# Optimization experiments

Measured on AMD Instinct MI355X. Metric: run time of the kernel, lower is better.

## Reference

```python
import jax, jax.numpy as jnp
import numpy as np

B, L, E, H, HID, V, C = 256, 64, 300, 100, 200, 30000, 3


def setup_inputs() -> dict:
    key = jax.random.key(0)
    ks = jax.random.split(key, 20)
    rep1 = jax.random.randint(ks[0], (B, L), 0, V)
    rep2 = jax.random.randint(ks[1], (B, L), 0, V)
    len1 = jax.random.randint(ks[2], (B,), 1, L + 1)
    len2 = jax.random.randint(ks[3], (B,), 1, L + 1)
    ar = jnp.arange(L)
    mask1 = (ar[None, :] < len1[:, None]).astype(jnp.float32)
    mask2 = (ar[None, :] < len2[:, None]).astype(jnp.float32)
    emb = jax.random.normal(ks[4], (V, E), jnp.float32) * 0.1
    k = 1.0 / np.sqrt(H)
    u = lambda kk, s, a: jax.random.uniform(kk, s, jnp.float32, -a, a)
    W_ih1 = u(ks[5], (4 * H, E), k); W_hh1 = u(ks[6], (4 * H, H), k)
    b_ih1 = u(ks[7], (4 * H,), k);   b_hh1 = u(ks[8], (4 * H,), k)
    W_ih2 = u(ks[9], (4 * H, E), k); W_hh2 = u(ks[10], (4 * H, H), k)
    b_ih2 = u(ks[11], (4 * H,), k);  b_hh2 = u(ks[12], (4 * H,), k)
    # attention params: module inits uniform(-0.5, 0.5)
    Wy = u(ks[13], (H, H), 0.5); Wh = u(ks[14], (H, H), 0.5)
    Wr = u(ks[15], (H, H), 0.5); Wp = u(ks[16], (H, H), 0.5)
    aW = u(ks[17], (1, H), 0.5)
    k1 = 1.0 / np.sqrt(2 * H)
    W1 = u(ks[18], (HID, 2 * H), k1); b1 = u(ks[18], (HID,), k1)
    k2 = 1.0 / np.sqrt(HID)
    W2 = u(ks[19], (C, HID), k2); b2 = u(ks[19], (C,), k2)
    return {"rep1": rep1, "len1": len1, "mask1": mask1,
            "rep2": rep2, "len2": len2, "mask2": mask2,
            "emb": emb,
            "W_ih1": W_ih1, "W_hh1": W_hh1, "b_ih1": b_ih1, "b_hh1": b_hh1,
            "W_ih2": W_ih2, "W_hh2": W_hh2, "b_ih2": b_ih2, "b_hh2": b_hh2,
            "Wy": Wy, "Wh": Wh, "Wr": Wr, "Wp": Wp, "aW": aW,
            "W1": W1, "b1": b1, "W2": W2, "b2": b2}


def reference(rep1, len1, mask1, rep2, len2, mask2, emb,
              W_ih1, W_hh1, b_ih1, b_hh1, W_ih2, W_hh2, b_ih2, b_hh2,
              Wy, Wh, Wr, Wp, aW, W1, b1, W2, b2):
    Bb = rep1.shape[0]
    Hh = Wy.shape[0]
    bidx = jnp.arange(Bb)

    def run_lstm(sen, h0, c0, Wih, Whh, bih, bhh):
        # sen: [L, B, E]; PyTorch LSTM gate order i, f, g, o
        def step(carry, x):
            h, c = carry
            g = x @ Wih.T + bih + h @ Whh.T + bhh
            i, f, gg, o = jnp.split(g, 4, axis=-1)
            c = jax.nn.sigmoid(f) * c + jax.nn.sigmoid(i) * jnp.tanh(gg)
            h = jax.nn.sigmoid(o) * jnp.tanh(c)
            return (h, c), (h, c)
        _, (hs, cs) = jax.lax.scan(step, (h0, c0), sen)
        return hs, cs  # [L, B, H]

    def get_rep(sen1, sen2, l1, m1, l2):
        z = jnp.zeros((Bb, Hh), sen1.dtype)
        hs, cs = run_lstm(sen1, z, z, W_ih1, W_hh1, b_ih1, b_hh1)
        outp = hs.transpose(1, 0, 2)                      # [B, L, H]
        h0 = outp[bidx, l1 - 1]                           # last valid h
        c0 = cs.transpose(1, 0, 2)[bidx, l1 - 1]          # last valid c
        hs2, _ = run_lstm(sen2, h0, c0, W_ih2, W_hh2, b_ih2, b_hh2)
        lstm_outs = hs2.transpose(1, 0, 2)                # [B, L, H]
        WyY = outp @ Wy                                   # [B, L, H]
        a = aW[0]

        def ctx_step(cv, h_t):
            # h_t: [B, H]; recurrent Wr term on previous context vector
            WhH = (h_t @ Wh + cv @ Wr)[:, None, :] * m1[:, :, None]
            M = jnp.tanh(WyY + WhH)                       # [B, L, H]
            s = jnp.einsum('blh,h->bl', M, a)
            e = jnp.exp(s - s.max(1, keepdims=True)) * m1  # masked softmax numerator
            attn = e / e.sum(1, keepdims=True)
            cv_new = jnp.einsum('bl,blh->bh', attn, outp)
            return cv_new, cv_new

        _, cvs = jax.lax.scan(ctx_step, z, hs2)           # [L, B, H]
        cv = cvs.transpose(1, 0, 2)[bidx, l2 - 1]
        lo = lstm_outs[bidx, l2 - 1]
        return jnp.tanh(cv @ Wp + lo @ Wh)

    s1 = emb[rep1].transpose(1, 0, 2)   # [L, B, E]
    s2 = emb[rep2].transpose(1, 0, 2)
    f1 = get_rep(s1, s2, len1, mask1, len2)
    f2 = get_rep(s2, s1, len2, mask2, len1)
    final = jnp.concatenate([f1, f2], axis=1)             # [B, 2H]
    fc = jnp.tanh(final @ W1.T + b1)                      # dropout_rate = 0
    logits = fc @ W2.T + b2
    return jax.nn.log_softmax(logits, axis=1)
```

## Files before the change

### kernel.cpp

```cpp
#include <hip/hip_runtime.h>
#include <math.h>


__device__ __forceinline__ float sigf(float x) { return 1.f / (1.f + expf(-x)); }

__device__ __forceinline__ unsigned short f2b(float f) {
    unsigned int u = __float_as_uint(f);
    unsigned int r = (u + 0x7FFFu + ((u >> 16) & 1u)) >> 16;
    return (unsigned short)r;
}

typedef __attribute__((ext_vector_type(8))) short short8v;
typedef __attribute__((ext_vector_type(4))) float float4v;

__global__ void f32_to_bf16_kernel(const float* __restrict__ in,
                                   unsigned short* __restrict__ out, int n4)
{
    int i = blockIdx.x * blockDim.x + threadIdx.x;
    int stride = gridDim.x * blockDim.x;
    for (; i < n4; i += stride) {
        float4 v = ((const float4*)in)[i];
        ushort4 b;
        b.x = f2b(v.x); b.y = f2b(v.y); b.z = f2b(v.z); b.w = f2b(v.w);
        ((ushort4*)out)[i] = b;
    }
}

__global__ __launch_bounds__(256)
void gemm_xproj_mfma(const unsigned short* __restrict__ embb,
                     const int* __restrict__ repA, const int* __restrict__ repB,
                     const float* __restrict__ W,
                     const float* __restrict__ bias1, const float* __restrict__ bias2,
                     float* __restrict__ out)
{
    __shared__ __align__(16) unsigned short Afr[512 * 8];
    __shared__ __align__(16) unsigned short Bfr[320 * 8];
    int tid = threadIdx.x;
    int m0 = blockIdx.x * 128;
    int n0 = blockIdx.y * 80;
    int lane = tid & 63, wave = tid >> 6;

    int sA0 = tid * 2, sA1 = sA0 + 1;
    int lA0 = sA0 & 63, lA1 = sA1 & 63;
    int rA0 = m0 + (sA0 >> 6) * 16 + (lA0 & 15);
    int rA1 = m0 + (sA1 >> 6) * 16 + (lA1 & 15);
    int kgA0 = (lA0 >> 4) * 8, kgA1 = (lA1 >> 4) * 8;
    int tt0 = rA0 >> 9, bb0 = rA0 & 511;
    int tok0 = (bb0 < 256) ? repA[bb0 * 64 + tt0] : repB[(bb0 - 256) * 64 + tt0];
    int tt1 = rA1 >> 9, bb1 = rA1 & 511;
    int tok1 = (bb1 < 256) ? repA[bb1 * 64 + tt1] : repB[(bb1 - 256) * 64 + tt1];
    const unsigned short* pa0 = embb + (size_t)tok0 * 300 + kgA0;
    const unsigned short* pa1 = embb + (size_t)tok1 * 300 + kgA1;

    int sB0 = tid;
    int nB0 = n0 + (sB0 >> 6) * 16 + (sB0 & 15);
    int kgB0 = ((sB0 & 63) >> 4) * 8;
    const float* pb0 = W + (size_t)nB0 * 300 + kgB0;
    int nB1 = n0 + 64 + (tid & 15);
    int kgB1 = (tid >> 4) * 8;
    const float* pb1 = W + (size_t)nB1 * 300 + kgB1;

    float4v acc[2][5];
#pragma unroll
    for (int i = 0; i < 2; i++)
#pragma unroll
        for (int j = 0; j < 5; j++) acc[i][j] = (float4v){0.f, 0.f, 0.f, 0.f};

    for (int k0 = 0; k0 < 300; k0 += 32) {
        {
            unsigned short* d = &Afr[sA0 * 8];
            int kk = k0 + kgA0;
            if (kk + 8 <= 300) {
                *(ushort4*)d = *(const ushort4*)(pa0 + k0);
                *(ushort4*)(d + 4) = *(const ushort4*)(pa0 + k0 + 4);
            } else {
#pragma unroll
                for (int i = 0; i < 8; i++) d[i] = (kk + i < 300) ? pa0[k0 + i] : 0;
            }
        }
        {
            unsigned short* d = &Afr[sA1 * 8];
            int kk = k0 + kgA1;
            if (kk + 8 <= 300) {
                *(ushort4*)d = *(const ushort4*)(pa1 + k0);
                *(ushort4*)(d + 4) = *(const ushort4*)(pa1 + k0 + 4);
            } else {
#pragma unroll
                for (int i = 0; i < 8; i++) d[i] = (kk + i < 300) ? pa1[k0 + i] : 0;
            }
        }
        {
            unsigned short* d = &Bfr[sB0 * 8];
            int kk = k0 + kgB0;
            if (kk + 8 <= 300) {
                float4 lo = *(const float4*)(pb0 + k0);
                float4 hi = *(const float4*)(pb0 + k0 + 4);
                d[0] = f2b(lo.x); d[1] = f2b(lo.y); d[2] = f2b(lo.z); d[3] = f2b(lo.w);
                d[4] = f2b(hi.x); d[5] = f2b(hi.y); d[6] = f2b(hi.z); d[7] = f2b(hi.w);
            } else {
#pragma unroll
                for (int i = 0; i < 8; i++) d[i] = (kk + i < 300) ? f2b(pb0[k0 + i]) : 0;
            }
        }
        if (tid < 64) {
            unsigned short* d = &Bfr[(256 + tid) * 8];
            int kk = k0 + kgB1;
            if (kk + 8 <= 300) {
                float4 lo = *(const float4*)(pb1 + k0);
                float4 hi = *(const float4*)(pb1 + k0 + 4);
                d[0] = f2b(lo.x); d[1] = f2b(lo.y); d[2] = f2b(lo.z); d[3] = f2b(lo.w);
                d[4] = f2b(hi.x); d[5] = f2b(hi.y); d[6] = f2b(hi.z); d[7] = f2b(hi.w);
            } else {
#pragma unroll
                for (int i = 0; i < 8; i++) d[i] = (kk + i < 300) ? f2b(pb1[k0 + i]) : 0;
            }
        }
        __syncthreads();
        short8v a0 = ((const short8v*)Afr)[(wave * 2 + 0) * 64 + lane];
        short8v a1 = ((const short8v*)Afr)[(wave * 2 + 1) * 64 + lane];
#pragma unroll
        for (int nt = 0; nt < 5; nt++) {
            short8v b = ((const short8v*)Bfr)[nt * 64 + lane];
            acc[0][nt] = __builtin_amdgcn_mfma_f32_16x16x32_bf16(a0, b, acc[0][nt], 0, 0, 0);
            acc[1][nt] = __builtin_amdgcn_mfma_f32_16x16x32_bf16(a1, b, acc[1][nt], 0, 0, 0);
        }
        __syncthreads();
    }

    int rbase = (lane >> 4) * 4;
    int cbase = lane & 15;
#pragma unroll
    for (int mtl = 0; mtl < 2; mtl++) {
        int mt = wave * 2 + mtl;
#pragma unroll
        for (int nt = 0; nt < 5; nt++) {
            int col = n0 + nt * 16 + cbase;
            float bsum = bias1[col] + bias2[col];
#pragma unroll
            for (int r = 0; r < 4; r++) {
                int row = m0 + mt * 16 + rbase + r;
                out[(size_t)row * 400 + col] = acc[mtl][nt][r] + bsum;
            }
        }
    }
}

template<int TRANSB, int TRANSOUT>
__global__ void gemm_kernel(const float* __restrict__ A,
                            const float* __restrict__ Bm,
                            float* __restrict__ out, int M, int N, int K, int lda)
{
    __shared__ float As[8][132];
    __shared__ float Bs[8][132];
    int tid = threadIdx.x;
    int m0 = blockIdx.x * 128;
    int n0 = blockIdx.y * 128;
    int tx = tid & 15, ty = tid >> 4;
    float acc[8][8];
#pragma unroll
    for (int i = 0; i < 8; i++)
#pragma unroll
        for (int j = 0; j < 8; j++) acc[i][j] = 0.f;

    int mr = m0 + (tid >> 1);
    int p = tid & 1;
    const float* arow = A + (size_t)mr * lda;

    for (int k0 = 0; k0 < K; k0 += 8) {
        int kk = k0 + p * 4;
        float4 av = make_float4(0.f, 0.f, 0.f, 0.f);
        if (kk + 3 < K) {
            av = *(const float4*)(arow + kk);
        } else {
            float tmp[4] = {0.f, 0.f, 0.f, 0.f};
            for (int i = 0; i < 4; i++) if (kk + i < K) tmp[i] = arow[kk + i];
            av = make_float4(tmp[0], tmp[1], tmp[2], tmp[3]);
        }
        int ml = tid >> 1;
        As[p * 4 + 0][ml] = av.x; As[p * 4 + 1][ml] = av.y;
        As[p * 4 + 2][ml] = av.z; As[p * 4 + 3][ml] = av.w;

        {
            int kl = tid >> 5;
            int nc = (tid & 31) * 4;
            int krow = k0 + kl;
            float4 bv = make_float4(0.f, 0.f, 0.f, 0.f);
            if (krow < K) {
                if (n0 + nc + 3 < N) {
                    bv = *(const float4*)(Bm + (size_t)krow * N + n0 + nc);
                } else {
                    float tmp[4] = {0.f, 0.f, 0.f, 0.f};
                    for (int i = 0; i < 4; i++) if (n0 + nc + i < N) tmp[i] = Bm[(size_t)krow * N + n0 + nc + i];
                    bv = make_float4(tmp[0], tmp[1], tmp[2], tmp[3]);
                }
            }
            Bs[kl][nc + 0] = bv.x; Bs[kl][nc + 1] = bv.y;
            Bs[kl][nc + 2] = bv.z; Bs[kl][nc + 3] = bv.w;
        }
        __syncthreads();
#pragma unroll
        for (int k = 0; k < 8; k++) {
            float4 a0 = *(const float4*)&As[k][ty * 8];
            float4 a1 = *(const float4*)&As[k][ty * 8 + 4];
            float4 b0 = *(const float4*)&Bs[k][tx * 8];
            float4 b1 = *(const float4*)&Bs[k][tx * 8 + 4];
            float am[8] = {a0.x, a0.y, a0.z, a0.w, a1.x, a1.y, a1.z, a1.w};
            float bn[8] = {b0.x, b0.y, b0.z, b0.w, b1.x, b1.y, b1.z, b1.w};
#pragma unroll
            for (int i = 0; i < 8; i++)
#pragma unroll
                for (int j = 0; j < 8; j++) acc[i][j] += am[i] * bn[j];
        }
        __syncthreads();
    }

#pragma unroll
    for (int i = 0; i < 8; i++) {
        int m = m0 + ty * 8 + i;
#pragma unroll
        for (int j = 0; j < 8; j++) {
            int n = n0 + tx * 8 + j;
            if (n < N) {
                size_t oi;
                if (TRANSOUT) oi = ((size_t)(m >> 6) * N + n) * 64 + (m & 63);
                else oi = (size_t)m * N + n;
                out[oi] = acc[i][j];
            }
        }
    }
}

__global__ __launch_bounds__(512, 2)
void lstm_kernel(const float* __restrict__ X, const float* __restrict__ Whh,
                 const float* __restrict__ hs_prev, const float* __restrict__ cs_prev,
                 const int* __restrict__ len1, const int* __restrict__ len2,
                 float* __restrict__ hs_out, float* __restrict__ cs_out)
{
    int t = threadIdx.x;
    int b0 = blockIdx.x * 2, b1 = b0 + 1;
    __shared__ float4 h0s4[25], h1s4[25];
    __shared__ float g0s[400], g1s[400];
    float* h0s = (float*)h0s4;
    float* h1s = (float*)h1s4;

    float4 w[25];
    if (t < 400) {
        const float* wr = Whh + t * 100;
#pragma unroll
        for (int i = 0; i < 25; i++) w[i] = ((const float4*)wr)[i];
    }
    float c0r = 0.f, c1r = 0.f;
    if (hs_prev) {
        if (t < 100) {
            int la = (b0 < 256) ? len1[b0] : len2[b0 - 256];
            h0s[t] = hs_prev[(b0 * 64 + la - 1) * 100 + t];
            c0r = cs_prev[(b0 * 64 + la - 1) * 100 + t];
        } else if (t < 200) {
            int j = t - 100;
            int la = (b1 < 256) ? len1[b1] : len2[b1 - 256];
            h1s[j] = hs_prev[(b1 * 64 + la - 1) * 100 + j];
            c1r = cs_prev[(b1 * 64 + la - 1) * 100 + j];
        }
    } else {
        if (t < 100) h0s[t] = 0.f;
        else if (t < 200) h1s[t - 100] = 0.f;
    }
    __syncthreads();

    for (int ts = 0; ts < 64; ts++) {
        if (t < 400) {
            float x0 = X[(ts * 512 + b0) * 400 + t];
            float x1 = X[(ts * 512 + b1) * 400 + t];
            float acc0a = 0.f, acc1a = 0.f;
            float acc0b = 0.f, acc1b = 0.f;
#pragma unroll
            for (int i = 0; i < 25; i++) {
                float4 hv0 = h0s4[i], hv1 = h1s4[i];
                acc0a += w[i].x * hv0.x + w[i].y * hv0.y;
                acc0b += w[i].z * hv0.z + w[i].w * hv0.w;
                acc1a += w[i].x * hv1.x + w[i].y * hv1.y;
                acc1b += w[i].z * hv1.z + w[i].w * hv1.w;
            }
            g0s[t] = acc0a + acc0b + x0;
            g1s[t] = acc1a + acc1b + x1;
        }
        __syncthreads();
        if (t < 200) {
            int j = (t < 100) ? t : t - 100;
            const float* gs = (t < 100) ? g0s : g1s;
            float ig = sigf(gs[j]);
            float fg = sigf(gs[100 + j]);
            float gg = tanhf(gs[200 + j]);
            float og = sigf(gs[300 + j]);
            float c = (t < 100) ? c0r : c1r;
            c = fg * c + ig * gg;
            float h = og * tanhf(c);
            if (t < 100) {
                c0r = c; h0s[j] = h;
                hs_out[(b0 * 64 + ts) * 100 + j] = h;
                if (cs_out) cs_out[(b0 * 64 + ts) * 100 + j] = c;
            } else {
                c1r = c; h1s[j] = h;
                hs_out[(b1 * 64 + ts) * 100 + j] = h;
                if (cs_out) cs_out[(b1 * 64 + ts) * 100 + j] = c;
            }
        }
        __syncthreads();
    }
}

__global__ __launch_bounds__(256, 2)
void attn_fast(const float* __restrict__ WyYT, const float* __restrict__ outp,
               const float* __restrict__ WhH, const float* __restrict__ Wr,
               const float* __restrict__ Wp, const float* __restrict__ aW,
               const float* __restrict__ mask1, const float* __restrict__ mask2,
               const int* __restrict__ len1, const int* __restrict__ len2,
               float* __restrict__ rep)
{
    int t = threadIdx.x;
    int bg = blockIdx.x;
    __shared__ __align__(16) float wyy2[64][100];
    __shared__ float whq2[100];
    __shared__ float atl[64];
    __shared__ __align__(16) float ucv[104];
    __shared__ float den[2];
    __shared__ float csel[100];

    int j = t >> 1, half = t & 1;
    int l3 = t >> 2, q3 = t & 3;

    const float* wy = WyYT + (size_t)bg * 6400;
    for (int idx = t; idx < 6400; idx += 256)
        wyy2[idx & 63][idx >> 6] = 2.f * wy[idx];

    const float* ob = outp + (size_t)bg * 6400;
    float oreg[32];
    if (t < 200) {
#pragma unroll
        for (int i = 0; i < 32; i++)
            oreg[i] = ob[(half * 32 + i) * 100 + j];
    }
    float wrreg[50];
    if (t < 200) {
#pragma unroll
        for (int k = 0; k < 50; k++)
            wrreg[k] = Wr[(half * 50 + k) * 100 + j];
    }
    float a2r[25];
#pragma unroll
    for (int i = 0; i < 25; i++) a2r[i] = 2.f * aW[q3 * 25 + i];
    float sumA;
    {
        float p = 0.f;
#pragma unroll
        for (int i = 0; i < 25; i++) p += a2r[i];
        p += __shfl_xor(p, 1);
        p += __shfl_xor(p, 2);
        sumA = 0.5f * p;
    }
    float m3 = (bg < 256) ? mask1[bg * 64 + l3] : mask2[(bg - 256) * 64 + l3];
    int lenB = (bg < 256) ? len2[bg] : len1[bg - 256];

    if (t < 104) ucv[t] = 0.f;
    if (t < 2) den[t] = 0.5f;

    const float* whrow = WhH + (size_t)bg * 6400;
    float whc = (t < 200) ? whrow[j] : 0.f;
    float densel = 1.f, uselreg = 0.f;
    __syncthreads();

    for (int ts = 0; ts < 64; ts++) {
        if (t < 200) {
            float dsum = den[0] + den[1];
            if (ts == lenB) densel = dsum;
            float rd = __builtin_amdgcn_rcpf(dsum);
            float whn = (ts < 63) ? whrow[(ts + 1) * 100 + j] : 0.f;
            float p0 = 0.f, p1 = 0.f;
            const float2* uc2 = (const float2*)(ucv + half * 50);
#pragma unroll
            for (int i = 0; i < 25; i++) {
                float2 c = uc2[i];
                p0 += wrreg[2 * i] * c.x;
                p1 += wrreg[2 * i + 1] * c.y;
            }
            float comb = p0 + p1;
            comb += __shfl_xor(comb, 1);
            if (!half) whq2[j] = 2.f * (whc + comb * rd);
            whc = whn;
        }
        __syncthreads();
        {
            const float* wyr = &wyy2[l3][q3 * 25];
            const float* wqp = &whq2[q3 * 25];
            float neg = 0.f;
#pragma unroll
            for (int i = 0; i < 25; i++) {
                float arg = wyr[i] + m3 * wqp[i];
                neg += a2r[i] * __builtin_amdgcn_rcpf(__expf(arg) + 1.f);
            }
            neg += __shfl_xor(neg, 1);
            neg += __shfl_xor(neg, 2);
            float e = __expf(sumA - neg) * m3;
            if (q3 == 0) atl[l3] = e;
        }
        __syncthreads();
        if (t < 200) {
            const float* al = &atl[half * 32];
            float p0 = 0.f, p1 = 0.f;
#pragma unroll
            for (int i = 0; i < 16; i++) {
                p0 += al[2 * i] * oreg[2 * i];
                p1 += al[2 * i + 1] * oreg[2 * i + 1];
            }
            float comb = p0 + p1;
            comb += __shfl_xor(comb, 1);
            if (ts == lenB - 1) uselreg = comb;
            if (!half) ucv[j] = comb;
        } else if (t < 202) {
            int hh = t - 200;
            const float* al = &atl[hh * 32];
            float d = 0.f;
#pragma unroll
            for (int i = 0; i < 32; i++) d += al[i];
            den[hh] = d;
        }
        __syncthreads();
    }

    if (lenB == 64 && t < 200) densel = den[0] + den[1];
    if (t < 200 && !half) csel[j] = uselreg * __builtin_amdgcn_rcpf(densel);
    __syncthreads();
    if (t < 100) {
        float r = whrow[(lenB - 1) * 100 + t];
#pragma unroll
        for (int k = 0; k < 100; k++) r += csel[k] * Wp[k * 100 + t];
        rep[(size_t)bg * 100 + t] = tanhf(r);
    }
}

__global__ void final_kernel(const float* __restrict__ rep,
                             const float* __restrict__ W1, const float* __restrict__ b1,
                             const float* __restrict__ W2, const float* __restrict__ b2,
                             float* __restrict__ out)
{
    int b = blockIdx.x;
    int t = threadIdx.x;
    __shared__ float4 fin4[50];
    __shared__ float4 fc4[50];
    __shared__ float lg[3];
    float* fin = (float*)fin4;
    float* fc = (float*)fc4;
    if (t < 200) fin[t] = (t < 100) ? rep[b * 100 + t] : rep[(b + 256) * 100 + (t - 100)];
    __syncthreads();
    if (t < 200) {
        float acc = b1[t];
        const float4* w = (const float4*)(W1 + t * 200);
#pragma unroll
        for (int k = 0; k < 50; k++) {
            float4 wv = w[k];
            float4 fv = fin4[k];
            acc += wv.x * fv.x + wv.y * fv.y + wv.z * fv.z + wv.w * fv.w;
        }
        fc[t] = tanhf(acc);
    }
    __syncthreads();
    if (t < 3) {
        float acc = b2[t];
        const float4* w = (const float4*)(W2 + t * 200);
        for (int k = 0; k < 50; k++) {
            float4 wv = w[k];
            float4 fv = fc4[k];
            acc += wv.x * fv.x + wv.y * fv.y + wv.z * fv.z + wv.w * fv.w;
        }
        lg[t] = acc;
    }
    __syncthreads();
    if (t == 0) {
        float m = fmaxf(lg[0], fmaxf(lg[1], lg[2]));
        float s = expf(lg[0] - m) + expf(lg[1] - m) + expf(lg[2] - m);
        float lse = m + logf(s);
        out[b * 3 + 0] = lg[0] - lse;
        out[b * 3 + 1] = lg[1] - lse;
        out[b * 3 + 2] = lg[2] - lse;
    }
}

extern "C" void kernel_launch(void* const* d_in, const int* in_sizes, int n_in,
                              void* d_out, int out_size, void* d_ws, size_t ws_size,
                              hipStream_t stream)
{
    const int*   rep1  = (const int*)d_in[0];
    const int*   len1  = (const int*)d_in[1];
    const float* mask1 = (const float*)d_in[2];
    const int*   rep2  = (const int*)d_in[3];
    const int*   len2  = (const int*)d_in[4];
    const float* mask2 = (const float*)d_in[5];
    const float* emb   = (const float*)d_in[6];
    const float* W_ih1 = (const float*)d_in[7];
    const float* W_hh1 = (const float*)d_in[8];
    const float* b_ih1 = (const float*)d_in[9];
    const float* b_hh1 = (const float*)d_in[10];
    const float* W_ih2 = (const float*)d_in[11];
    const float* W_hh2 = (const float*)d_in[12];
    const float* b_ih2 = (const float*)d_in[13];
    const float* b_hh2 = (const float*)d_in[14];
    const float* Wy    = (const float*)d_in[15];
    const float* Wh    = (const float*)d_in[16];
    const float* Wr    = (const float*)d_in[17];
    const float* Wp    = (const float*)d_in[18];
    const float* aW    = (const float*)d_in[19];
    const float* W1    = (const float*)d_in[20];
    const float* b1    = (const float*)d_in[21];
    const float* W2    = (const float*)d_in[22];
    const float* b2    = (const float*)d_in[23];

    float* ws = (float*)d_ws;
    float* X    = ws;
    float* hs1  = X + 13107200;
    float* cs1  = hs1 + 3276800;
    float* hs2  = cs1 + 3276800;
    float* WyYT = hs2 + 3276800;
    float* rep  = WyYT + 3276800;
    unsigned short* embb = (unsigned short*)hs2;

    dim3 gm(256, 5);
    dim3 gw(256, 1);

    f32_to_bf16_kernel<<<1024, 256, 0, stream>>>(emb, embb, 2250000);
    gemm_xproj_mfma<<<gm, 256, 0, stream>>>(embb, rep1, rep2, W_ih1, b_ih1, b_hh1, X);
    lstm_kernel<<<256, 512, 0, stream>>>(X, W_hh1, nullptr, nullptr, nullptr, nullptr, hs1, cs1);
    gemm_xproj_mfma<<<gm, 256, 0, stream>>>(embb, rep2, rep1, W_ih2, b_ih2, b_hh2, X);
    gemm_kernel<1, 1><<<gw, 256, 0, stream>>>(hs1, Wy, WyYT, 32768, 100, 100, 100);
    lstm_kernel<<<256, 512, 0, stream>>>(X, W_hh2, hs1, cs1, len1, len2, hs2, nullptr);
    gemm_kernel<1, 0><<<gw, 256, 0, stream>>>(hs2, Wh, X, 32768, 100, 100, 100);
    attn_fast<<<512, 256, 0, stream>>>(WyYT, hs1, X, Wr, Wp, aW,
                                       mask1, mask2, len1, len2, rep);
    final_kernel<<<256, 256, 0, stream>>>(rep, W1, b1, W2, b2, (float*)d_out);
}
```

Measured before the change: 717.9 us.

## Restructure LSTM recurrence to one sequence per block with wave-shuffle gate exchange

Replaces the two-sequences-per-block LSTM kernel with one sequence per block, where each wavefront holds the four gate rows of 16 hidden units. Gates move between lanes with shuffles instead of a shared gate buffer, and a double-buffered hidden state drops one barrier per timestep. The next timestep's input projection is prefetched into a register, and fast exp/rcp versions of sigmoid and tanh are used. This doubles the block count and reduces synchronization on the serial recurrence, at the cost of slightly lower transcendental accuracy and some idle lanes in the last wave.

```diff
diff --git a/kernel.cpp b/kernel.cpp
--- a/kernel.cpp
+++ b/kernel.cpp
@@ -3,6 +3,8 @@
 
 
 __device__ __forceinline__ float sigf(float x) { return 1.f / (1.f + expf(-x)); }
+__device__ __forceinline__ float fsig(float x) { return __builtin_amdgcn_rcpf(1.f + __expf(-x)); }
+__device__ __forceinline__ float ftanh(float x) { return 1.f - 2.f * __builtin_amdgcn_rcpf(__expf(2.f * x) + 1.f); }
 
 __device__ __forceinline__ unsigned short f2b(float f) {
     unsigned int u = __float_as_uint(f);
@@ -230,82 +232,78 @@
     }
 }
 
-__global__ __launch_bounds__(512, 2)
-void lstm_kernel(const float* __restrict__ X, const float* __restrict__ Whh,
-                 const float* __restrict__ hs_prev, const float* __restrict__ cs_prev,
-                 const int* __restrict__ len1, const int* __restrict__ len2,
-                 float* __restrict__ hs_out, float* __restrict__ cs_out)
+__global__ __launch_bounds__(512)
+void lstm_wave(const float* __restrict__ X, const float* __restrict__ Whh,
+               const float* __restrict__ hs_prev, const float* __restrict__ cs_prev,
+               const int* __restrict__ len1, const int* __restrict__ len2,
+               float* __restrict__ hs_out, float* __restrict__ cs_out)
 {
     int t = threadIdx.x;
-    int b0 = blockIdx.x * 2, b1 = b0 + 1;
-    __shared__ float4 h0s4[25], h1s4[25];
-    __shared__ float g0s[400], g1s[400];
-    float* h0s = (float*)h0s4;
-    float* h1s = (float*)h1s4;
+    int bg = blockIdx.x;
+    int lane = t & 63;
+    int wave = t >> 6;
+    int sub = lane & 15;
+    int q = lane >> 4;
+    int e = wave * 16 + sub;
+    bool act = e < 100;
+    int ew = act ? e : 0;
+
+    __shared__ __align__(16) float hbuf[2][104];
 
     float4 w[25];
-    if (t < 400) {
-        const float* wr = Whh + t * 100;
-#pragma unroll
-        for (int i = 0; i < 25; i++) w[i] = ((const float4*)wr)[i];
-    }
-    float c0r = 0.f, c1r = 0.f;
+    {
+        const float4* wr = (const float4*)(Whh + (size_t)(q * 100 + ew) * 100);
+#pragma unroll
+        for (int i = 0; i < 25; i++) w[i] = wr[i];
+    }
+
+    float c = 0.f;
     if (hs_prev) {
-        if (t < 100) {
-            int la = (b0 < 256) ? len1[b0] : len2[b0 - 256];
-            h0s[t] = hs_prev[(b0 * 64 + la - 1) * 100 + t];
-            c0r = cs_prev[(b0 * 64 + la - 1) * 100 + t];
-        } else if (t < 200) {
-            int j = t - 100;
-            int la = (b1 < 256) ? len1[b1] : len2[b1 - 256];
-            h1s[j] = hs_prev[(b1 * 64 + la - 1) * 100 + j];
-            c1r = cs_prev[(b1 * 64 + la - 1) * 100 + j];
-        }
+        int la = (bg < 256) ? len1[bg] : len2[bg - 256];
+        size_t off = ((size_t)bg * 64 + la - 1) * 100 + ew;
+        c = cs_prev[off];
+        if (act && q == 0) hbuf[0][e] = hs_prev[off];
     } else {
-        if (t < 100) h0s[t] = 0.f;
-        else if (t < 200) h1s[t - 100] = 0.f;
-    }
+        if (act && q == 0) hbuf[0][e] = 0.f;
+    }
+
+    const float* xp = X + (size_t)bg * 400 + (q * 100 + ew);
+    float xv = xp[0];
+    float* hs_row = hs_out + (size_t)bg * 6400;
+    float* cs_row = cs_out ? (cs_out + (size_t)bg * 6400) : nullptr;
     __syncthreads();
 
     for (int ts = 0; ts < 64; ts++) {
-        if (t < 400) {
-            float x0 = X[(ts * 512 + b0) * 400 + t];
-            float x1 = X[(ts * 512 + b1) * 400 + t];
-            float acc0a = 0.f, acc1a = 0.f;
-            float acc0b = 0.f, acc1b = 0.f;
-#pragma unroll
-            for (int i = 0; i < 25; i++) {
-                float4 hv0 = h0s4[i], hv1 = h1s4[i];
-                acc0a += w[i].x * hv0.x + w[i].y * hv0.y;
-                acc0b += w[i].z * hv0.z + w[i].w * hv0.w;
-                acc1a += w[i].x * hv1.x + w[i].y * hv1.y;
-                acc1b += w[i].z * hv1.z + w[i].w * hv1.w;
-            }
-            g0s[t] = acc0a + acc0b + x0;
-            g1s[t] = acc1a + acc1b + x1;
-        }
-        __syncthreads();
-        if (t < 200) {
-            int j = (t < 100) ? t : t - 100;
-            const float* gs = (t < 100) ? g0s : g1s;
-            float ig = sigf(gs[j]);
-            float fg = sigf(gs[100 + j]);
-            float gg = tanhf(gs[200 + j]);
-            float og = sigf(gs[300 + j]);
-            float c = (t < 100) ? c0r : c1r;
-            c = fg * c + ig * gg;
-            float h = og * tanhf(c);
-            if (t < 100) {
-                c0r = c; h0s[j] = h;
-                hs_out[(b0 * 64 + ts) * 100 + j] = h;
-                if (cs_out) cs_out[(b0 * 64 + ts) * 100 + j] = c;
-            } else {
-                c1r = c; h1s[j] = h;
-                hs_out[(b1 * 64 + ts) * 100 + j] = h;
-                if (cs_out) cs_out[(b1 * 64 + ts) * 100 + j] = c;
-            }
-        }
-        __syncthreads();
+        float xn = 0.f;
+        if (ts < 63) xn = xp[(size_t)(ts + 1) * 204800];
+        const float4* h4 = (const float4*)hbuf[ts & 1];
+        float a0 = 0.f, a1 = 0.f, a2 = 0.f, a3 = 0.f;
+#pragma unroll
+        for (int i = 0; i < 24; i += 4) {
+            float4 h0 = h4[i], h1 = h4[i + 1], h2 = h4[i + 2], h3 = h4[i + 3];
+            a0 += w[i].x * h0.x + w[i].y * h0.y + w[i].z * h0.z + w[i].w * h0.w;
+            a1 += w[i+1].x * h1.x + w[i+1].y * h1.y + w[i+1].z * h1.z + w[i+1].w * h1.w;
+            a2 += w[i+2].x * h2.x + w[i+2].y * h2.y + w[i+2].z * h2.z + w[i+2].w * h2.w;
+            a3 += w[i+3].x * h3.x + w[i+3].y * h3.y + w[i+3].z * h3.z + w[i+3].w * h3.w;
+        }
+        {
+            float4 h0 = h4[24];
+            a0 += w[24].x * h0.x + w[24].y * h0.y + w[24].z * h0.z + w[24].w * h0.w;
+        }
+        float gv = (a0 + a1) + (a2 + a3) + xv;
+        float gi = __shfl(gv, sub);
+        float gf = __shfl(gv, sub + 16);
+        float gg = __shfl(gv, sub + 32);
+        float go = __shfl(gv, sub + 48);
+        c = fsig(gf) * c + fsig(gi) * ftanh(gg);
+        float h = fsig(go) * ftanh(c);
+        if (act && q == 0) {
+            hbuf[(ts + 1) & 1][e] = h;
+            hs_row[ts * 100 + e] = h;
+            if (cs_row) cs_row[ts * 100 + e] = c;
+        }
+        __syncthreads();
+        xv = xn;
     }
 }
 
@@ -379,9 +377,9 @@
             const float2* uc2 = (const float2*)(ucv + half * 50);
 #pragma unroll
             for (int i = 0; i < 25; i++) {
-                float2 c = uc2[i];
-                p0 += wrreg[2 * i] * c.x;
-                p1 += wrreg[2 * i + 1] * c.y;
+                float2 cc = uc2[i];
+                p0 += wrreg[2 * i] * cc.x;
+                p1 += wrreg[2 * i + 1] * cc.y;
             }
             float comb = p0 + p1;
             comb += __shfl_xor(comb, 1);
@@ -528,10 +526,10 @@
 
     f32_to_bf16_kernel<<<1024, 256, 0, stream>>>(emb, embb, 2250000);
     gemm_xproj_mfma<<<gm, 256, 0, stream>>>(embb, rep1, rep2, W_ih1, b_ih1, b_hh1, X);
-    lstm_kernel<<<256, 512, 0, stream>>>(X, W_hh1, nullptr, nullptr, nullptr, nullptr, hs1, cs1);
+    lstm_wave<<<512, 512, 0, stream>>>(X, W_hh1, nullptr, nullptr, nullptr, nullptr, hs1, cs1);
     gemm_xproj_mfma<<<gm, 256, 0, stream>>>(embb, rep2, rep1, W_ih2, b_ih2, b_hh2, X);
     gemm_kernel<1, 1><<<gw, 256, 0, stream>>>(hs1, Wy, WyYT, 32768, 100, 100, 100);
-    lstm_kernel<<<256, 512, 0, stream>>>(X, W_hh2, hs1, cs1, len1, len2, hs2, nullptr);
+    lstm_wave<<<512, 512, 0, stream>>>(X, W_hh2, hs1, cs1, len1, len2, hs2, nullptr);
     gemm_kernel<1, 0><<<gw, 256, 0, stream>>>(hs2, Wh, X, 32768, 100, 100, 100);
     attn_fast<<<512, 256, 0, stream>>>(WyYT, hs1, X, Wr, Wp, aW,
                                        mask1, mask2, len1, len2, rep);
```

Result: faster. 678.5 us (-5.5%).
